# Kernel optimization log

Measured on AMD Instinct MI355X. Metric: run time of the kernel, lower is better.

## Reference

```python
import jax, jax.numpy as jnp
import numpy as np

B, T, D = 64, 512, 1024  # batch, step_dim, feature_dim


def setup_inputs() -> dict:
    key = jax.random.key(0)
    k1, k2, k3, k4, k5 = jax.random.split(key, 5)
    x = jax.random.normal(k1, (B, T, D), dtype=jnp.float32)
    mask = jax.random.randint(k2, (B, T), 0, 2).astype(bool)
    mask = mask.at[:, 0].set(True)  # guarantee >=1 valid token per row
    # xavier_uniform bounds
    w_bound = float(np.sqrt(6.0 / (D + D)))
    c_bound = float(np.sqrt(6.0 / (T + 1)))
    weight = jax.random.uniform(k3, (D, D), minval=-w_bound, maxval=w_bound, dtype=jnp.float32)
    context_vector = jax.random.uniform(k4, (T, 1), minval=-c_bound, maxval=c_bound, dtype=jnp.float32)
    b = jnp.zeros((T,), dtype=jnp.float32)
    return {"x": x, "mask": mask, "weight": weight, "context_vector": context_vector, "b": b}


def reference(x, mask, weight, context_vector, b):
    # batched bilinear scores: eij[b,t,s] = x[b,t,:] @ W @ x[b,s,:]^T
    xw = jnp.einsum('btd,de->bte', x, weight)          # [B,T,D]
    eij = jnp.einsum('bte,bse->bts', xw, x)            # [B,T,T]
    # bias over last axis (matches view(-1, T) + b), tanh
    eij = jnp.tanh(eij + b)                            # [B,T,T]
    # context-vector reduction over last axis -> [B,T]
    scores = jnp.einsum('bts,s->bt', eij, context_vector[:, 0])
    # masked softmax over T
    scores = jnp.where(mask, scores, -jnp.inf)
    a = jax.nn.softmax(scores, axis=1)                 # [B,T]
    # weighted sum of inputs -> [B,D]
    out = jnp.einsum('btd,bt->bd', x, a)
    return (out, a)
```

## Files before the change

kernel.cpp:

```cpp
#include <hip/hip_runtime.h>
#include <hip/hip_bf16.h>
#include <math.h>

#define B_ 64
#define T_ 512
#define D_ 1024
#define M_ (B_*T_)

typedef unsigned short u16;
typedef __attribute__((ext_vector_type(8))) _Float16 f16x8;
typedef __attribute__((ext_vector_type(4))) float f32x4;

__device__ __forceinline__ u16 f2h(float f) {
  union { _Float16 h; u16 u; } v;
  v.h = (_Float16)f;
  return v.u;
}

__device__ __forceinline__ float h2f(u16 u) {
  union { u16 u; _Float16 h; } v;
  v.u = u;
  return (float)v.h;
}

__device__ __forceinline__ float fast_tanh(float x) {
  return 1.0f - 2.0f / (__expf(2.0f * x) + 1.0f);
}

__device__ __forceinline__ void gll16(const void* g, void* l) {
  __builtin_amdgcn_global_load_lds(
      (const __attribute__((address_space(1))) unsigned int*)g,
      (__attribute__((address_space(3))) unsigned int*)l, 16, 0, 0);
}

__global__ __launch_bounds__(256) void cvt_x_kernel(const float4* __restrict__ x,
                                                    ushort4* __restrict__ xh, int n4) {
  int i = blockIdx.x * 256 + threadIdx.x;
  if (i < n4) {
    float4 v = x[i];
    ushort4 o;
    o.x = f2h(v.x); o.y = f2h(v.y); o.z = f2h(v.z); o.w = f2h(v.w);
    xh[i] = o;
  }
}

__global__ __launch_bounds__(1024) void cvt_wt_kernel(const float* __restrict__ W,
                                                      u16* __restrict__ Wt) {
  __shared__ float tile[32][33];
  int tx = threadIdx.x & 31, ty = threadIdx.x >> 5;
  int n0 = blockIdx.x * 32, k0 = blockIdx.y * 32;
  tile[ty][tx] = W[(k0 + ty) * D_ + n0 + tx];
  __syncthreads();
  Wt[(n0 + ty) * D_ + k0 + tx] = f2h(tile[tx][ty]);
}


__device__ __forceinline__ void gemm_core256(const u16* __restrict__ Abase,
                                             const u16* __restrict__ Bbase, int K,
                                             u16* As, u16* Bs, int tid, f32x4 acc[8][4]) {
  const int wave = tid >> 6, lane = tid & 63;
  const int swz_c = ((lane & 3) - ((lane >> 3) & 3)) & 3;
  const int rin = lane >> 2;
  const u16* gA[4]; u16* lA[4];
#pragma unroll
  for (int j = 0; j < 4; j++) {
    int ci = wave * 4 + j;
    gA[j] = Abase + (long)(ci * 16 + rin) * K + swz_c * 8;
    lA[j] = As + ci * 512;
  }
  const u16* gB[2]; u16* lB[2];
#pragma unroll
  for (int j = 0; j < 2; j++) {
    int ci = wave * 2 + j;
    gB[j] = Bbase + (long)(ci * 16 + rin) * K + swz_c * 8;
    lB[j] = Bs + ci * 512;
  }

  const int wrow = (wave >> 1) * 128, wcol = (wave & 1) * 64;
  const int lm = lane & 15, qd = lane >> 4;
  const int swz_r = ((qd + (lm >> 1)) & 3) * 8;
  const u16* ra = As + (wrow + lm) * 32 + swz_r;
  const u16* rb = Bs + (wcol + lm) * 32 + swz_r;

  for (int kt = 0; kt < K; kt += 32) {
#pragma unroll
    for (int j = 0; j < 4; j++) { gll16(gA[j], lA[j]); gA[j] += 32; }
#pragma unroll
    for (int j = 0; j < 2; j++) { gll16(gB[j], lB[j]); gB[j] += 32; }
    __syncthreads();
    f16x8 af[8], bfr[4];
#pragma unroll
    for (int i = 0; i < 8; i++) af[i] = *(const f16x8*)(ra + i * 512);
#pragma unroll
    for (int i = 0; i < 4; i++) bfr[i] = *(const f16x8*)(rb + i * 512);
#pragma unroll
    for (int mi = 0; mi < 8; mi++)
#pragma unroll
      for (int ni = 0; ni < 4; ni++)
        acc[mi][ni] = __builtin_amdgcn_mfma_f32_16x16x32_f16(af[mi], bfr[ni], acc[mi][ni], 0, 0, 0);
    __syncthreads();
  }
}

__device__ __forceinline__ void gemm_core128(const u16* __restrict__ Abase,
                                             const u16* __restrict__ Bbase, int K,
                                             u16* As, u16* Bs, int tid, f32x4 acc[4][4]) {
  const int wave = tid >> 6, lane = tid & 63;
  const int swz_c = ((lane & 3) - ((lane >> 3) & 3)) & 3;
  const int rin = lane >> 2;
  const u16* gA[2]; u16* lA[2];
  const u16* gB[2]; u16* lB[2];
#pragma unroll
  for (int j = 0; j < 2; j++) {
    int ci = wave * 2 + j;
    gA[j] = Abase + (long)(ci * 16 + rin) * K + swz_c * 8;
    lA[j] = As + ci * 512;
    gB[j] = Bbase + (long)(ci * 16 + rin) * K + swz_c * 8;
    lB[j] = Bs + ci * 512;
  }
  const int wrow = (wave >> 1) * 64, wcol = (wave & 1) * 64;
  const int lm = lane & 15, qd = lane >> 4;
  const int swz_r = ((qd + (lm >> 1)) & 3) * 8;
  const u16* ra = As + (wrow + lm) * 32 + swz_r;
  const u16* rb = Bs + (wcol + lm) * 32 + swz_r;

  for (int kt = 0; kt < K; kt += 32) {
#pragma unroll
    for (int j = 0; j < 2; j++) {
      gll16(gA[j], lA[j]); gA[j] += 32;
      gll16(gB[j], lB[j]); gB[j] += 32;
    }
    __syncthreads();
    f16x8 af[4], bfr[4];
#pragma unroll
    for (int i = 0; i < 4; i++) {
      af[i] = *(const f16x8*)(ra + i * 512);
      bfr[i] = *(const f16x8*)(rb + i * 512);
    }
#pragma unroll
    for (int mi = 0; mi < 4; mi++)
#pragma unroll
      for (int ni = 0; ni < 4; ni++)
        acc[mi][ni] = __builtin_amdgcn_mfma_f32_16x16x32_f16(af[mi], bfr[ni], acc[mi][ni], 0, 0, 0);
    __syncthreads();
  }
}

__global__ __launch_bounds__(256, 2) void gemm1_kernel(const u16* __restrict__ xh,
                                                       const u16* __restrict__ wt,
                                                       u16* __restrict__ xw) {
  __shared__ u16 As[256 * 32], Bs[128 * 32];
  f32x4 acc[8][4] = {};
  const int tid = threadIdx.x;
  const int bx = blockIdx.x;
  const int xcd = bx & 7, j = bx >> 3;
  const int mt = xcd * 16 + (j >> 3);
  const int nt = j & 7;
  const long m0 = (long)mt * 256;
  const long n0 = (long)nt * 128;
  gemm_core256(xh + m0 * D_, wt + n0 * D_, D_, As, Bs, tid, acc);

  const int wave = tid >> 6, lane = tid & 63;
  const int wrow = (wave >> 1) * 128, wcol = (wave & 1) * 64;
  const int lm = lane & 15, qd = lane >> 4;
#pragma unroll
  for (int mi = 0; mi < 8; mi++)
#pragma unroll
    for (int ni = 0; ni < 4; ni++) {
      long m = m0 + wrow + mi * 16 + qd * 4;
      long n = n0 + wcol + ni * 16 + lm;
      u16* p = xw + m * D_ + n;
#pragma unroll
      for (int r = 0; r < 4; r++) p[(long)r * D_] = f2h(acc[mi][ni][r]);
    }
}

__global__ __launch_bounds__(256, 4) void gemm2_kernel(const u16* __restrict__ xw,
                                                       const u16* __restrict__ xh,
                                                       const float* __restrict__ bias,
                                                       const float* __restrict__ cv,
                                                       float* __restrict__ scores_part) {
  __shared__ u16 As[128 * 32], Bs[128 * 32];
  f32x4 acc[4][4] = {};
  const int bx = blockIdx.x;
  const int xcd = bx & 7, j = bx >> 3;
  const int bb = xcd * 8 + (j >> 4);
  const int tile = j & 15;
  const int tt = tile >> 2, st = tile & 3;
  const int tid = threadIdx.x;
  const long arow = (long)bb * T_ + tt * 128;
  const long brow = (long)bb * T_ + st * 128;
  gemm_core128(xw + arow * D_, xh + brow * D_, D_, As, Bs, tid, acc);

  const int wave = tid >> 6, lane = tid & 63;
  const int wrow = (wave >> 1) * 64, wcol = (wave & 1) * 64;
  const int lm = lane & 15, qd = lane >> 4;
  float cvv[4], bv[4];
#pragma unroll
  for (int ni = 0; ni < 4; ni++) {
    int s = st * 128 + wcol + ni * 16 + lm;
    cvv[ni] = cv[s];
    bv[ni] = bias[s];
  }
  const int plane = st * 2 + (wave & 1);
  float* dst = scores_part + plane * (B_ * T_) + bb * T_ + tt * 128;
#pragma unroll
  for (int mi = 0; mi < 4; mi++) {
#pragma unroll
    for (int r = 0; r < 4; r++) {
      float p = 0.f;
#pragma unroll
      for (int ni = 0; ni < 4; ni++) p += fast_tanh(acc[mi][ni][r] + bv[ni]) * cvv[ni];
      p += __shfl_xor(p, 1); p += __shfl_xor(p, 2);
      p += __shfl_xor(p, 4); p += __shfl_xor(p, 8);
      if (lm == 0) dst[wrow + mi * 16 + qd * 4 + r] = p;
    }
  }
}

__global__ __launch_bounds__(512) void softmax_kernel(const float* __restrict__ sp,
                                                      const unsigned char* __restrict__ m8,
                                                      float* __restrict__ a_out) {
  const int b = blockIdx.x, t = threadIdx.x;
  __shared__ int nonz;
  __shared__ float redm[8], reds[8];
  if (t == 0) nonz = 0;
  __syncthreads();
  unsigned char c = m8[t * 4 + 1] | m8[t * 4 + 2] | m8[t * 4 + 3];
  if (c) atomicOr(&nonz, 1);
  __syncthreads();
  const bool is_i32 = (nonz == 0);
  const int idx = b * T_ + t;
  const bool valid = is_i32 ? (m8[(long)idx * 4] != 0) : (m8[idx] != 0);

  float val = 0.f;
#pragma unroll
  for (int pl = 0; pl < 8; pl++) val += sp[pl * (B_ * T_) + idx];
  if (!valid) val = -INFINITY;
  float m = val;
#pragma unroll
  for (int o = 32; o > 0; o >>= 1) m = fmaxf(m, __shfl_xor(m, o));
  const int wv = t >> 6, ln = t & 63;
  if (ln == 0) redm[wv] = m;
  __syncthreads();
  float rowmax = redm[0];
#pragma unroll
  for (int i = 1; i < 8; i++) rowmax = fmaxf(rowmax, redm[i]);

  float e = valid ? expf(val - rowmax) : 0.f;
  float ssum = e;
#pragma unroll
  for (int o = 32; o > 0; o >>= 1) ssum += __shfl_xor(ssum, o);
  if (ln == 0) reds[wv] = ssum;
  __syncthreads();
  float tot = 0.f;
#pragma unroll
  for (int i = 0; i < 8; i++) tot += reds[i];
  a_out[idx] = e / tot;
}

__global__ __launch_bounds__(256) void wsum_kernel(const u16* __restrict__ xh,
                                                   const float* __restrict__ a,
                                                   float* __restrict__ out) {
  const int b = blockIdx.x, sl = blockIdx.y, tid = threadIdx.x;
  const int d = sl * 256 + tid;
  const u16* xp = xh + (long)b * T_ * D_ + d;
  const float* ap = a + b * T_;
  float acc = 0.f;
  for (int t = 0; t < T_; t++)
    acc += ap[t] * h2f(xp[(long)t * D_]);
  out[(long)b * D_ + d] = acc;
}

extern "C" void kernel_launch(void* const* d_in, const int* in_sizes, int n_in,
                              void* d_out, int out_size, void* d_ws, size_t ws_size,
                              hipStream_t stream) {
  const float* x = (const float*)d_in[0];
  const unsigned char* mask = (const unsigned char*)d_in[1];
  const float* W = (const float*)d_in[2];
  const float* cv = (const float*)d_in[3];
  const float* bias = (const float*)d_in[4];

  float* out = (float*)d_out;
  float* a_out = out + (size_t)B_ * D_;

  char* ws = (char*)d_ws;
  u16* xh = (u16*)(ws);
  u16* wt = (u16*)(ws + 67108864);
  float* scores_part = (float*)(ws + 67108864);
  u16* xw = (u16*)(ws + 69206016);

  cvt_x_kernel<<<(M_ * D_ / 4 + 255) / 256, 256, 0, stream>>>((const float4*)x,
                                                              (ushort4*)xh, M_ * D_ / 4);
  cvt_wt_kernel<<<dim3(32, 32), 1024, 0, stream>>>(W, wt);
  gemm1_kernel<<<1024, 256, 0, stream>>>(xh, wt, xw);
  gemm2_kernel<<<1024, 256, 0, stream>>>(xw, xh, bias, cv, scores_part);
  softmax_kernel<<<B_, 512, 0, stream>>>(scores_part, mask, a_out);
  wsum_kernel<<<dim3(B_, 4), 256, 0, stream>>>(xh, a_out, out);
}
```

Before: 342.7 us.

## Shrink gemm1 tiles to 128x128 and vectorize wsum with split-T reduction

gemm1 now uses the 128x128 core with 2048 blocks and a four-blocks-per-CU launch bound in place of the 256x128 tile, trading per-block reuse for more occupancy and parallelism. wsum_kernel now has each thread load four fp16 values at a time. The four waves each cover a quarter of T and combine their partial sums through shared memory, which raises memory parallelism and cuts the serial loop length. The smaller GEMM tile raises operand reload traffic from global memory.

```diff
diff --git a/kernel.cpp b/kernel.cpp
--- a/kernel.cpp
+++ b/kernel.cpp
@@ -55,53 +55,6 @@
 }
 
 
-__device__ __forceinline__ void gemm_core256(const u16* __restrict__ Abase,
-                                             const u16* __restrict__ Bbase, int K,
-                                             u16* As, u16* Bs, int tid, f32x4 acc[8][4]) {
-  const int wave = tid >> 6, lane = tid & 63;
-  const int swz_c = ((lane & 3) - ((lane >> 3) & 3)) & 3;
-  const int rin = lane >> 2;
-  const u16* gA[4]; u16* lA[4];
-#pragma unroll
-  for (int j = 0; j < 4; j++) {
-    int ci = wave * 4 + j;
-    gA[j] = Abase + (long)(ci * 16 + rin) * K + swz_c * 8;
-    lA[j] = As + ci * 512;
-  }
-  const u16* gB[2]; u16* lB[2];
-#pragma unroll
-  for (int j = 0; j < 2; j++) {
-    int ci = wave * 2 + j;
-    gB[j] = Bbase + (long)(ci * 16 + rin) * K + swz_c * 8;
-    lB[j] = Bs + ci * 512;
-  }
-
-  const int wrow = (wave >> 1) * 128, wcol = (wave & 1) * 64;
-  const int lm = lane & 15, qd = lane >> 4;
-  const int swz_r = ((qd + (lm >> 1)) & 3) * 8;
-  const u16* ra = As + (wrow + lm) * 32 + swz_r;
-  const u16* rb = Bs + (wcol + lm) * 32 + swz_r;
-
-  for (int kt = 0; kt < K; kt += 32) {
-#pragma unroll
-    for (int j = 0; j < 4; j++) { gll16(gA[j], lA[j]); gA[j] += 32; }
-#pragma unroll
-    for (int j = 0; j < 2; j++) { gll16(gB[j], lB[j]); gB[j] += 32; }
-    __syncthreads();
-    f16x8 af[8], bfr[4];
-#pragma unroll
-    for (int i = 0; i < 8; i++) af[i] = *(const f16x8*)(ra + i * 512);
-#pragma unroll
-    for (int i = 0; i < 4; i++) bfr[i] = *(const f16x8*)(rb + i * 512);
-#pragma unroll
-    for (int mi = 0; mi < 8; mi++)
-#pragma unroll
-      for (int ni = 0; ni < 4; ni++)
-        acc[mi][ni] = __builtin_amdgcn_mfma_f32_16x16x32_f16(af[mi], bfr[ni], acc[mi][ni], 0, 0, 0);
-    __syncthreads();
-  }
-}
-
 __device__ __forceinline__ void gemm_core128(const u16* __restrict__ Abase,
                                              const u16* __restrict__ Bbase, int K,
                                              u16* As, u16* Bs, int tid, f32x4 acc[4][4]) {
@@ -146,25 +99,25 @@
   }
 }
 
-__global__ __launch_bounds__(256, 2) void gemm1_kernel(const u16* __restrict__ xh,
+__global__ __launch_bounds__(256, 4) void gemm1_kernel(const u16* __restrict__ xh,
                                                        const u16* __restrict__ wt,
                                                        u16* __restrict__ xw) {
-  __shared__ u16 As[256 * 32], Bs[128 * 32];
-  f32x4 acc[8][4] = {};
+  __shared__ u16 As[128 * 32], Bs[128 * 32];
+  f32x4 acc[4][4] = {};
   const int tid = threadIdx.x;
   const int bx = blockIdx.x;
   const int xcd = bx & 7, j = bx >> 3;
-  const int mt = xcd * 16 + (j >> 3);
+  const int mt = xcd * 32 + (j >> 3);
   const int nt = j & 7;
-  const long m0 = (long)mt * 256;
+  const long m0 = (long)mt * 128;
   const long n0 = (long)nt * 128;
-  gemm_core256(xh + m0 * D_, wt + n0 * D_, D_, As, Bs, tid, acc);
+  gemm_core128(xh + m0 * D_, wt + n0 * D_, D_, As, Bs, tid, acc);
 
   const int wave = tid >> 6, lane = tid & 63;
-  const int wrow = (wave >> 1) * 128, wcol = (wave & 1) * 64;
+  const int wrow = (wave >> 1) * 64, wcol = (wave & 1) * 64;
   const int lm = lane & 15, qd = lane >> 4;
 #pragma unroll
-  for (int mi = 0; mi < 8; mi++)
+  for (int mi = 0; mi < 4; mi++)
 #pragma unroll
     for (int ni = 0; ni < 4; ni++) {
       long m = m0 + wrow + mi * 16 + qd * 4;
@@ -262,14 +215,31 @@
 __global__ __launch_bounds__(256) void wsum_kernel(const u16* __restrict__ xh,
                                                    const float* __restrict__ a,
                                                    float* __restrict__ out) {
-  const int b = blockIdx.x, sl = blockIdx.y, tid = threadIdx.x;
-  const int d = sl * 256 + tid;
-  const u16* xp = xh + (long)b * T_ * D_ + d;
+  __shared__ float4 lred[4][64];
+  const int b = blockIdx.x, dq = blockIdx.y, tid = threadIdx.x;
+  const int w = tid >> 6, lane = tid & 63;
+  const int d0 = dq * 256 + lane * 4;
+  const u16* xp = xh + (long)b * T_ * D_ + d0;
   const float* ap = a + b * T_;
-  float acc = 0.f;
-  for (int t = 0; t < T_; t++)
-    acc += ap[t] * h2f(xp[(long)t * D_]);
-  out[(long)b * D_ + d] = acc;
+  float4 acc = make_float4(0.f, 0.f, 0.f, 0.f);
+  for (int i = 0; i < 128; i++) {
+    int t = w * 128 + i;
+    float av = ap[t];
+    ushort4 xv = *(const ushort4*)(xp + (long)t * D_);
+    acc.x += av * h2f(xv.x); acc.y += av * h2f(xv.y);
+    acc.z += av * h2f(xv.z); acc.w += av * h2f(xv.w);
+  }
+  lred[w][lane] = acc;
+  __syncthreads();
+  if (w == 0) {
+    float4 s0 = lred[0][lane], s1 = lred[1][lane], s2 = lred[2][lane], s3 = lred[3][lane];
+    float4 s;
+    s.x = s0.x + s1.x + s2.x + s3.x;
+    s.y = s0.y + s1.y + s2.y + s3.y;
+    s.z = s0.z + s1.z + s2.z + s3.z;
+    s.w = s0.w + s1.w + s2.w + s3.w;
+    *(float4*)(out + (long)b * D_ + d0) = s;
+  }
 }
 
 extern "C" void kernel_launch(void* const* d_in, const int* in_sizes, int n_in,
@@ -293,7 +263,7 @@
   cvt_x_kernel<<<(M_ * D_ / 4 + 255) / 256, 256, 0, stream>>>((const float4*)x,
                                                               (ushort4*)xh, M_ * D_ / 4);
   cvt_wt_kernel<<<dim3(32, 32), 1024, 0, stream>>>(W, wt);
-  gemm1_kernel<<<1024, 256, 0, stream>>>(xh, wt, xw);
+  gemm1_kernel<<<2048, 256, 0, stream>>>(xh, wt, xw);
   gemm2_kernel<<<1024, 256, 0, stream>>>(xw, xh, bias, cv, scores_part);
   softmax_kernel<<<B_, 512, 0, stream>>>(scores_part, mask, a_out);
   wsum_kernel<<<dim3(B_, 4), 256, 0, stream>>>(xh, a_out, out);
```

Result: no change. 344.4 us (+0.5%).
